# Kernel tuning notes

Hardware: AMD Instinct MI355X
Metric: run time of the kernel (lower is better)

## Reference

```python
import jax, jax.numpy as jnp
import numpy as np

B, C, T = 128, 16, 2048
H = 256            # hidden_size
G = 4 * H          # gate dim (i, f, g, o in torch order)
NUM_OUT = 10


def setup_inputs() -> dict:
    key = jax.random.key(0)
    ks = jax.random.split(key, 7)
    s = 1.0 / np.sqrt(H)  # torch default LSTM init scale
    return {
        "x": jax.random.normal(ks[0], (B, C, T), dtype=jnp.float32),
        "w_ih": jax.random.uniform(ks[1], (G, C), minval=-s, maxval=s, dtype=jnp.float32),
        "w_hh": jax.random.uniform(ks[2], (G, H), minval=-s, maxval=s, dtype=jnp.float32),
        "b_ih": jax.random.uniform(ks[3], (G,), minval=-s, maxval=s, dtype=jnp.float32),
        "b_hh": jax.random.uniform(ks[4], (G,), minval=-s, maxval=s, dtype=jnp.float32),
        "w_out": jax.random.uniform(ks[5], (NUM_OUT, H), minval=-s, maxval=s, dtype=jnp.float32),
        "b_out": jax.random.uniform(ks[6], (NUM_OUT,), minval=-s, maxval=s, dtype=jnp.float32),
    }


def _lstm_last_hidden(x, w_ih, w_hh, b_ih, b_hh):
    # x: (B, C, T) -> (B, T, C)
    xt = jnp.swapaxes(x, 1, 2)
    # Precompute input projections for all timesteps: (B, T, 4H)
    xproj = jnp.einsum('btc,gc->btg', xt, w_ih) + b_ih + b_hh
    xs = jnp.swapaxes(xproj, 0, 1)  # (T, B, 4H) for scan

    h0 = jnp.zeros((xt.shape[0], w_hh.shape[1]), dtype=x.dtype)
    c0 = jnp.zeros_like(h0)

    def step(carry, xp):
        h, cell = carry
        gates = xp + h @ w_hh.T               # (B, 4H)
        i, f, g, o = jnp.split(gates, 4, axis=-1)  # torch gate order i,f,g,o
        i = jax.nn.sigmoid(i)
        f = jax.nn.sigmoid(f)
        g = jnp.tanh(g)
        o = jax.nn.sigmoid(o)
        cell = f * cell + i * g
        h = o * jnp.tanh(cell)
        return (h, cell), None

    (hT, _), _ = jax.lax.scan(step, (h0, c0), xs)
    return hT  # (B, H): hidden state at last timestep


def reference(x, w_ih, w_hh, b_ih, b_hh, w_out, b_out):
    # bn0 is Identity (c.normalize_data=True)
    hT = _lstm_last_hidden(x, w_ih, w_hh, b_ih, b_hh)
    logits = hT @ w_out.T + b_out  # (B, num_outputs)
    return jax.nn.log_softmax(logits, axis=1)
```

## Files before the change

kernel.cpp:

```cpp
#include <hip/hip_runtime.h>
#include <cstdint>
#include <cstddef>

#define NB 128
#define NC 16
#define NT 2048
#define NH 256
#define NG 1024
#define NO 10

typedef _Float16 f16;
typedef _Float16 h2 __attribute__((ext_vector_type(2)));
typedef _Float16 h8 __attribute__((ext_vector_type(8)));
typedef int i32x4 __attribute__((ext_vector_type(4)));
typedef long long2_ __attribute__((ext_vector_type(2)));

static __device__ __forceinline__ float fdot2(h2 a, h2 b, float c) {
#if __has_builtin(__builtin_amdgcn_fdot2)
  return __builtin_amdgcn_fdot2(a, b, c, false);
#else
  return c + (float)a[0] * (float)b[0] + (float)a[1] * (float)b[1];
#endif
}

static __device__ __forceinline__ int sdot4(int a, int b, int c) {
#if __has_builtin(__builtin_amdgcn_sdot4)
  return __builtin_amdgcn_sdot4(a, b, c, false);
#else
  int r = c;
#pragma unroll
  for (int i = 0; i < 4; ++i)
    r += (int)(int8_t)(a >> (8 * i)) * (int)(int8_t)(b >> (8 * i));
  return r;
#endif
}

static __device__ __forceinline__ i32x4 mfma_i8_k64(i32x4 a, i32x4 b, i32x4 c) {
#if __has_builtin(__builtin_amdgcn_mfma_i32_16x16x64_i8)
  return __builtin_amdgcn_mfma_i32_16x16x64_i8(a, b, c, 0, 0, 0);
#else
  long2_ al = __builtin_bit_cast(long2_, a);
  long2_ bl = __builtin_bit_cast(long2_, b);
  c = __builtin_amdgcn_mfma_i32_16x16x32_i8(al[0], bl[0], c, 0, 0, 0);
  c = __builtin_amdgcn_mfma_i32_16x16x32_i8(al[1], bl[1], c, 0, 0, 0);
  return c;
#endif
}

static __device__ __forceinline__ float pairswap(float v) {
  int r = __builtin_amdgcn_update_dpp(0, __builtin_bit_cast(int, v),
                                      0xB1, 0xF, 0xF, true);
  return __builtin_bit_cast(float, r);
}

static __device__ __forceinline__ float sigm(float x) {
  return __builtin_amdgcn_rcpf(1.f + __expf(-x));
}
static __device__ __forceinline__ float tanh_(float x) {
  return 1.f - 2.f * __builtin_amdgcn_rcpf(1.f + __expf(2.f * x));
}

__global__ void prepack_whh_i8(const float* __restrict__ whh,
                               int8_t* __restrict__ wq,
                               float* __restrict__ scale) {
  int row = blockIdx.x;
  int k   = threadIdx.x;
  float v = whh[row * NH + k];
  float m = fabsf(v);
  for (int off = 32; off; off >>= 1) m = fmaxf(m, __shfl_xor(m, off, 64));
  __shared__ float smax[4];
  if ((k & 63) == 0) smax[k >> 6] = m;
  __syncthreads();
  float mm = fmaxf(fmaxf(smax[0], smax[1]), fmaxf(smax[2], smax[3]));
  float s = fmaxf(mm, 1e-20f) / 127.f;
  int qv = (int)rintf(v / s);
  qv = min(127, max(-127, qv));
  wq[row * NH + k] = (int8_t)qv;
  if (k == 0) scale[row] = s;
}

__global__ __launch_bounds__(512, 2)
void lstm_main(const float* __restrict__ x,
               const float* __restrict__ w_ih,
               const float* __restrict__ b_ih,
               const float* __restrict__ b_hh,
               const float* __restrict__ w_out,
               const float* __restrict__ b_out,
               const int8_t* __restrict__ wq,
               const float* __restrict__ scales,
               float* __restrict__ out) {
  const int t = threadIdx.x;
  const int l = t & 63;
  const int w = t >> 6;
  const int b = blockIdx.x;

  __shared__ __align__(16) int8_t hq[2][NH];
  __shared__ __align__(16) f16 xs[64][NC];
  __shared__ float hT[NH];
  __shared__ float lg[NO];

  ((int8_t*)hq)[t] = 0;
#pragma unroll
  for (int r = 0; r < 2; ++r) {
    int e = t + 512 * r;
    int cc = e >> 6, tt = e & 63;
    xs[tt][cc] = (f16)x[(size_t)(b * NC + cc) * NT + tt];
  }
  __syncthreads();

  const float K = 1.f / 127.f;

  if (w < 4) {
    const int row16 = l & 15;
    const int grp = l >> 4;
    const int sel = grp & 1;
    const int uu = 32 * w + 16 * sel + row16;

    i32x4 bw[4][2][4];
#pragma unroll
    for (int gt = 0; gt < 4; ++gt)
#pragma unroll
      for (int hf = 0; hf < 2; ++hf) {
        const int8_t* rp =
            wq + (size_t)(256 * gt + 32 * w + 16 * hf + row16) * NH + grp * 16;
#pragma unroll
        for (int kt = 0; kt < 4; ++kt)
          bw[gt][hf][kt] = *(const i32x4*)(rp + kt * 64);
      }

    h2 wih[4][8];
#pragma unroll
    for (int gt = 0; gt < 4; ++gt) {
      const float* rp = w_ih + (size_t)(256 * gt + uu) * NC;
#pragma unroll
      for (int q = 0; q < 8; ++q) {
        h2 t2 = {(f16)rp[2 * q], (f16)rp[2 * q + 1]};
        wih[gt][q] = t2;
      }
    }
    float sc[4], bb[4];
#pragma unroll
    for (int gt = 0; gt < 4; ++gt) {
      sc[gt] = scales[256 * gt + uu] * K;
      bb[gt] = b_ih[256 * gt + uu] + b_hh[256 * gt + uu];
    }

    float c_ = 0.f, h_last = 0.f;
#pragma unroll 1
    for (int s = 0; s < NT; ++s) {
      const int p = s & 1;
      const int8_t* hp = hq[p] + grp * 16;
      i32x4 a_[4];
#pragma unroll
      for (int kt = 0; kt < 4; ++kt) a_[kt] = *(const i32x4*)(hp + kt * 64);

      h8 xlo = *(const h8*)&xs[s & 63][0];
      h8 xhi = *(const h8*)&xs[s & 63][8];
      float xp[4];
#pragma unroll
      for (int gt = 0; gt < 4; ++gt) {
        float acc = bb[gt];
#pragma unroll
        for (int q = 0; q < 4; ++q) {
          h2 xa = {xlo[2 * q], xlo[2 * q + 1]};
          acc = fdot2(xa, wih[gt][q], acc);
        }
#pragma unroll
        for (int q = 0; q < 4; ++q) {
          h2 xa = {xhi[2 * q], xhi[2 * q + 1]};
          acc = fdot2(xa, wih[gt][q + 4], acc);
        }
        xp[gt] = acc;
      }

      float gv[4];
#pragma unroll
      for (int gt = 0; gt < 4; ++gt) {
        i32x4 a0 = {0, 0, 0, 0}, a1 = {0, 0, 0, 0};
#pragma unroll
        for (int kt = 0; kt < 4; ++kt) a0 = mfma_i8_k64(a_[kt], bw[gt][0][kt], a0);
#pragma unroll
        for (int kt = 0; kt < 4; ++kt) a1 = mfma_i8_k64(a_[kt], bw[gt][1][kt], a1);
        int d = sel ? a1[0] : a0[0];
        gv[gt] = xp[gt] + (float)d * sc[gt];
      }

      float ig = sigm(gv[0]);
      float fg = sigm(gv[1]);
      float gg = tanh_(gv[2]);
      float og = sigm(gv[3]);
      c_ = fg * c_ + ig * gg;
      float hh = og * tanh_(c_);
      h_last = hh;
      if (l < 32) hq[1 - p][uu] = (int8_t)(int)rintf(hh * 127.f);

      if ((s & 63) == 63 && s != NT - 1) {
        __syncthreads();
#pragma unroll
        for (int r = 0; r < 2; ++r) {
          int e = t + 512 * r;
          int cc = e >> 6, tt = e & 63;
          xs[tt][cc] = (f16)x[(size_t)(b * NC + cc) * NT + (s + 1) + tt];
        }
      }
      __syncthreads();
    }
    if (l < 32) hT[uu] = h_last;
  } else {
    const int q = l >> 1;
    const int half = l & 1;
    const int uv = 128 + 32 * (w - 4) + q;

    int wi_[32], wf_[32], wg_[32], wo_[32];
    {
      const int4* pi = (const int4*)(wq + (size_t)uv * NH + 128 * half);
      const int4* pf = (const int4*)(wq + (size_t)(256 + uv) * NH + 128 * half);
      const int4* pg = (const int4*)(wq + (size_t)(512 + uv) * NH + 128 * half);
      const int4* po = (const int4*)(wq + (size_t)(768 + uv) * NH + 128 * half);
#pragma unroll
      for (int c = 0; c < 8; ++c) {
        int4 vi = pi[c], vf = pf[c], vg = pg[c], vo = po[c];
        wi_[4 * c + 0] = vi.x; wi_[4 * c + 1] = vi.y; wi_[4 * c + 2] = vi.z; wi_[4 * c + 3] = vi.w;
        wf_[4 * c + 0] = vf.x; wf_[4 * c + 1] = vf.y; wf_[4 * c + 2] = vf.z; wf_[4 * c + 3] = vf.w;
        wg_[4 * c + 0] = vg.x; wg_[4 * c + 1] = vg.y; wg_[4 * c + 2] = vg.z; wg_[4 * c + 3] = vg.w;
        wo_[4 * c + 0] = vo.x; wo_[4 * c + 1] = vo.y; wo_[4 * c + 2] = vo.z; wo_[4 * c + 3] = vo.w;
      }
    }
    h2 wihv[4][4];
#pragma unroll
    for (int g4 = 0; g4 < 4; ++g4) {
      int row = uv + 256 * g4;
#pragma unroll
      for (int uu2 = 0; uu2 < 4; ++uu2) {
        h2 t2 = {(f16)w_ih[row * NC + 8 * half + 2 * uu2],
                 (f16)w_ih[row * NC + 8 * half + 2 * uu2 + 1]};
        wihv[g4][uu2] = t2;
      }
    }
    float sci = scales[uv] * K;
    float scf = scales[256 + uv] * K;
    float scg = scales[512 + uv] * K;
    float sco = scales[768 + uv] * K;
    float bi_ = half ? 0.f : b_ih[uv] + b_hh[uv];
    float bf_ = half ? 0.f : b_ih[256 + uv] + b_hh[256 + uv];
    float bg_ = half ? 0.f : b_ih[512 + uv] + b_hh[512 + uv];
    float bo_ = half ? 0.f : b_ih[768 + uv] + b_hh[768 + uv];

    float c_ = 0.f, h_last = 0.f;
#pragma unroll 1
    for (int s = 0; s < NT; ++s) {
      const int p = s & 1;
      const int4* hrd = (const int4*)(hq[p] + 128 * half);

      float fi = bi_, ff = bf_, fg_ = bg_, fo = bo_;
      {
        h8 xv = *(const h8*)&xs[s & 63][8 * half];
#pragma unroll
        for (int uu2 = 0; uu2 < 4; ++uu2) {
          h2 xp = {xv[2 * uu2], xv[2 * uu2 + 1]};
          fi = fdot2(xp, wihv[0][uu2], fi);
          ff = fdot2(xp, wihv[1][uu2], ff);
          fg_ = fdot2(xp, wihv[2][uu2], fg_);
          fo = fdot2(xp, wihv[3][uu2], fo);
        }
      }

      int ai = 0, af = 0, ag = 0, ao = 0;
#pragma unroll
      for (int c = 0; c < 8; ++c) {
        int4 hv = hrd[c];
        ai = sdot4(hv.x, wi_[4 * c + 0], ai); ai = sdot4(hv.y, wi_[4 * c + 1], ai);
        ai = sdot4(hv.z, wi_[4 * c + 2], ai); ai = sdot4(hv.w, wi_[4 * c + 3], ai);
        af = sdot4(hv.x, wf_[4 * c + 0], af); af = sdot4(hv.y, wf_[4 * c + 1], af);
        af = sdot4(hv.z, wf_[4 * c + 2], af); af = sdot4(hv.w, wf_[4 * c + 3], af);
        ag = sdot4(hv.x, wg_[4 * c + 0], ag); ag = sdot4(hv.y, wg_[4 * c + 1], ag);
        ag = sdot4(hv.z, wg_[4 * c + 2], ag); ag = sdot4(hv.w, wg_[4 * c + 3], ag);
        ao = sdot4(hv.x, wo_[4 * c + 0], ao); ao = sdot4(hv.y, wo_[4 * c + 1], ao);
        ao = sdot4(hv.z, wo_[4 * c + 2], ao); ao = sdot4(hv.w, wo_[4 * c + 3], ao);
      }

      float vi = fi + (float)ai * sci;
      float vf = ff + (float)af * scf;
      float vg = fg_ + (float)ag * scg;
      float vo = fo + (float)ao * sco;
      vi += pairswap(vi); vf += pairswap(vf); vg += pairswap(vg); vo += pairswap(vo);

      float ig = sigm(vi);
      float fgate = sigm(vf);
      float gv = tanh_(vg);
      float og = sigm(vo);
      c_ = fgate * c_ + ig * gv;
      float hh = og * tanh_(c_);
      h_last = hh;
      if (!half) hq[1 - p][uv] = (int8_t)(int)rintf(hh * 127.f);

      if ((s & 63) == 63 && s != NT - 1) {
        __syncthreads();
#pragma unroll
        for (int r = 0; r < 2; ++r) {
          int e = t + 512 * r;
          int cc = e >> 6, tt = e & 63;
          xs[tt][cc] = (f16)x[(size_t)(b * NC + cc) * NT + (s + 1) + tt];
        }
      }
      __syncthreads();
    }
    if (!half) hT[uv] = h_last;
  }

  __syncthreads();
  if (t < NO) {
    float acc = b_out[t];
    for (int k = 0; k < NH; ++k) acc += hT[k] * w_out[t * NH + k];
    lg[t] = acc;
  }
  __syncthreads();
  if (t == 0) {
    float m = lg[0];
    for (int o = 1; o < NO; ++o) m = fmaxf(m, lg[o]);
    float ssum = 0.f;
    for (int o = 0; o < NO; ++o) ssum += __expf(lg[o] - m);
    float lse = m + __logf(ssum);
    for (int o = 0; o < NO; ++o) out[b * NO + o] = lg[o] - lse;
  }
}

extern "C" void kernel_launch(void* const* d_in, const int* in_sizes, int n_in,
                              void* d_out, int out_size, void* d_ws, size_t ws_size,
                              hipStream_t stream) {
  const float* x    = (const float*)d_in[0];
  const float* wih  = (const float*)d_in[1];
  const float* whh  = (const float*)d_in[2];
  const float* bih  = (const float*)d_in[3];
  const float* bhh  = (const float*)d_in[4];
  const float* wout = (const float*)d_in[5];
  const float* bout = (const float*)d_in[6];
  float* out = (float*)d_out;
  int8_t* wq = (int8_t*)d_ws;
  float* scales = (float*)((char*)d_ws + NG * NH);

  hipLaunchKernelGGL(prepack_whh_i8, dim3(NG), dim3(NH), 0, stream, whh, wq, scales);
  hipLaunchKernelGGL(lstm_main, dim3(NB), dim3(512), 0, stream,
                     x, wih, bih, bhh, wout, bout, wq, scales, out);
}
```

Baseline: 1.993 ms.

## Assign MFMA and VALU wave roles by SIMD id and prioritize MFMA issue

Each wave reads its hardware SIMD id and claims a role (MFMA-based or VALU dot-product) through shared-memory counters, so that every SIMD holds one wave of each type instead of relying on the fixed wave-index split. The MFMA path also issues all eight int8 MFMA chains up front under raised scheduling priority, then does the fp16 input projection afterwards. The goal is to overlap matrix-core and vector work on each SIMD within the serial per-timestep recurrence. The cost is extra setup atomics and a dependence on how hardware ids map to SIMDs; if waves land unevenly, the fallback role swap keeps four waves per role.

```diff
diff --git a/kernel.cpp b/kernel.cpp
--- a/kernel.cpp
+++ b/kernel.cpp
@@ -98,7 +98,12 @@
   __shared__ __align__(16) f16 xs[64][NC];
   __shared__ float hT[NH];
   __shared__ float lg[NO];
-
+  __shared__ int sctr[4];
+  __shared__ int rctr[2];
+  __shared__ int role_of[8], blk_of[8];
+
+  if (t < 4) sctr[t] = 0;
+  if (t >= 4 && t < 6) rctr[t - 4] = 0;
   ((int8_t*)hq)[t] = 0;
 #pragma unroll
   for (int r = 0; r < 2; ++r) {
@@ -108,13 +113,31 @@
   }
   __syncthreads();
 
+  if (l == 0) {
+    unsigned hwid;
+    asm volatile("s_getreg_b32 %0, hwreg(HW_REG_HW_ID)" : "=s"(hwid));
+    int sid = (hwid >> 4) & 3;
+    int fst = atomicAdd(&sctr[sid], 1);
+    int role = fst & 1;
+    int blk = atomicAdd(&rctr[role], 1);
+    if (blk >= 4) {
+      role ^= 1;
+      blk = atomicAdd(&rctr[role], 1);
+    }
+    role_of[w] = role;
+    blk_of[w] = blk;
+  }
+  __syncthreads();
+  const int role = role_of[w];
+  const int blk = blk_of[w];
+
   const float K = 1.f / 127.f;
 
-  if (w < 4) {
+  if (role == 0) {
     const int row16 = l & 15;
     const int grp = l >> 4;
     const int sel = grp & 1;
-    const int uu = 32 * w + 16 * sel + row16;
+    const int uu = 32 * blk + 16 * sel + row16;
 
     i32x4 bw[4][2][4];
 #pragma unroll
@@ -122,7 +145,7 @@
 #pragma unroll
       for (int hf = 0; hf < 2; ++hf) {
         const int8_t* rp =
-            wq + (size_t)(256 * gt + 32 * w + 16 * hf + row16) * NH + grp * 16;
+            wq + (size_t)(256 * gt + 32 * blk + 16 * hf + row16) * NH + grp * 16;
 #pragma unroll
         for (int kt = 0; kt < 4; ++kt)
           bw[gt][hf][kt] = *(const i32x4*)(rp + kt * 64);
@@ -154,35 +177,38 @@
 #pragma unroll
       for (int kt = 0; kt < 4; ++kt) a_[kt] = *(const i32x4*)(hp + kt * 64);
 
+      __builtin_amdgcn_s_setprio(1);
+      i32x4 acc[4][2];
+#pragma unroll
+      for (int gt = 0; gt < 4; ++gt)
+#pragma unroll
+        for (int hf = 0; hf < 2; ++hf) {
+          i32x4 ac = {0, 0, 0, 0};
+#pragma unroll
+          for (int kt = 0; kt < 4; ++kt)
+            ac = mfma_i8_k64(a_[kt], bw[gt][hf][kt], ac);
+          acc[gt][hf] = ac;
+        }
+      __builtin_amdgcn_s_setprio(0);
+
       h8 xlo = *(const h8*)&xs[s & 63][0];
       h8 xhi = *(const h8*)&xs[s & 63][8];
-      float xp[4];
+      float gv[4];
 #pragma unroll
       for (int gt = 0; gt < 4; ++gt) {
-        float acc = bb[gt];
+        float acc_x = bb[gt];
 #pragma unroll
         for (int q = 0; q < 4; ++q) {
           h2 xa = {xlo[2 * q], xlo[2 * q + 1]};
-          acc = fdot2(xa, wih[gt][q], acc);
+          acc_x = fdot2(xa, wih[gt][q], acc_x);
         }
 #pragma unroll
         for (int q = 0; q < 4; ++q) {
           h2 xa = {xhi[2 * q], xhi[2 * q + 1]};
-          acc = fdot2(xa, wih[gt][q + 4], acc);
-        }
-        xp[gt] = acc;
-      }
-
-      float gv[4];
-#pragma unroll
-      for (int gt = 0; gt < 4; ++gt) {
-        i32x4 a0 = {0, 0, 0, 0}, a1 = {0, 0, 0, 0};
-#pragma unroll
-        for (int kt = 0; kt < 4; ++kt) a0 = mfma_i8_k64(a_[kt], bw[gt][0][kt], a0);
-#pragma unroll
-        for (int kt = 0; kt < 4; ++kt) a1 = mfma_i8_k64(a_[kt], bw[gt][1][kt], a1);
-        int d = sel ? a1[0] : a0[0];
-        gv[gt] = xp[gt] + (float)d * sc[gt];
+          acc_x = fdot2(xa, wih[gt][q + 4], acc_x);
+        }
+        int d = sel ? acc[gt][1][0] : acc[gt][0][0];
+        gv[gt] = acc_x + (float)d * sc[gt];
       }
 
       float ig = sigm(gv[0]);
@@ -209,7 +235,7 @@
   } else {
     const int q = l >> 1;
     const int half = l & 1;
-    const int uv = 128 + 32 * (w - 4) + q;
+    const int uv = 128 + 32 * blk + q;
 
     int wi_[32], wf_[32], wg_[32], wo_[32];
     {
```

Result: faster. 1.868 ms (-6.3%).
